# Optimization experiments

Hardware: AMD Instinct MI355X
Metric: run time of the kernel (lower is better)

## Reference

```python
import jax, jax.numpy as jnp
import numpy as np

B, S, H = 32, 2048, 1024

def setup_inputs() -> dict:
    key = jax.random.key(0)
    ks = jax.random.split(key, 8)
    scale = 1.0 / np.sqrt(H)
    return {
        "decoder_hidden": jax.random.normal(ks[0], (B, 1, H), dtype=jnp.float32),
        "encoder_outputs": jax.random.normal(ks[1], (B, S, H), dtype=jnp.float32),
        "coverage": jax.random.uniform(ks[2], (B, S), dtype=jnp.float32),
        "W_enc": jax.random.normal(ks[3], (H, H), dtype=jnp.float32) * scale,  # enc_v.weight [out,in]
        "W_dec": jax.random.normal(ks[4], (H, H), dtype=jnp.float32) * scale,  # dec_v.weight
        "b_dec": jax.random.normal(ks[5], (H,), dtype=jnp.float32) * scale,    # dec_v.bias
        "w_cov": jax.random.normal(ks[6], (H,), dtype=jnp.float32) * scale,    # cov_v.weight [H,1] squeezed
        "v": jax.random.normal(ks[7], (H,), dtype=jnp.float32) * scale,        # V_prime.weight [1,H] squeezed
    }

def reference(decoder_hidden, encoder_outputs, coverage, W_enc, W_dec, b_dec, w_cov, v):
    # enc_feature: [B,S,H]; torch Linear is x @ W.T
    enc_feature = jnp.einsum("bsh,oh->bso", encoder_outputs, W_enc)
    # dec_feature: [B,1,H], broadcasts over S
    dec_feature = jnp.einsum("bqh,oh->bqo", decoder_hidden, W_dec) + b_dec
    # cov_feature: coverage[...,None] @ w_cov[None,:] -> [B,S,H]
    cov_feature = coverage[..., None] * w_cov
    scores = jnp.tanh(enc_feature + dec_feature + cov_feature)  # [B,S,H]
    attn_scores = jnp.einsum("bsh,h->bs", scores, v)            # V_prime, squeeze(-1)
    attn_dist = jax.nn.softmax(attn_scores, axis=-1)[:, None, :]  # [B,1,S]
    return attn_dist
```

## Files before the change

### kernel.cpp

```cpp
#include <hip/hip_runtime.h>
#include <hip/hip_bf16.h>

#define Bb 32
#define Ss 2048
#define Hh 1024

typedef __attribute__((ext_vector_type(4))) float f32x4;
typedef __attribute__((ext_vector_type(8))) short s16x8;

#define GAS const __attribute__((address_space(1))) unsigned int
#define LAS __attribute__((address_space(3))) unsigned int

__device__ __forceinline__ unsigned short f2bf(float x) {
  unsigned int u = __float_as_uint(x);
  u = (u + 0x7fffu + ((u >> 16) & 1u)) >> 16;
  return (unsigned short)u;
}

__global__ void cvt_w_kernel(const float* __restrict__ W, unsigned short* __restrict__ out) {
  int g = blockIdx.x * blockDim.x + threadIdx.x;
  int o = g >> 7;
  int kc8 = (g & 127) << 3;
  const float4* src = reinterpret_cast<const float4*>(W + (size_t)o * Hh + kc8);
  float4 a = src[0], b = src[1];
  union { unsigned short u[8]; uint4 q; } rr;
  rr.u[0] = f2bf(a.x); rr.u[1] = f2bf(a.y); rr.u[2] = f2bf(a.z); rr.u[3] = f2bf(a.w);
  rr.u[4] = f2bf(b.x); rr.u[5] = f2bf(b.y); rr.u[6] = f2bf(b.z); rr.u[7] = f2bf(b.w);
  int ot = o >> 8, r = o & 255, kt = kc8 >> 6, kc = kc8 & 63;
  size_t byte = (size_t)(ot * 16 + kt) * 32768 + (size_t)((r * 128 + kc * 2) ^ ((r & 7) << 4));
  *reinterpret_cast<uint4*>(reinterpret_cast<char*>(out) + byte) = rr.q;
}

__global__ void dec_feat_kernel(const float* __restrict__ dh,
                                const float* __restrict__ Wd,
                                const float* __restrict__ bd,
                                float* __restrict__ out) {
  int gw = blockIdx.x * 4 + (threadIdx.x >> 6);
  int lane = threadIdx.x & 63;
  int b = gw >> 10;
  int o = gw & 1023;
  const float4* x = reinterpret_cast<const float4*>(dh + (size_t)b * Hh);
  const float4* w = reinterpret_cast<const float4*>(Wd + (size_t)o * Hh);
  float acc = 0.f;
#pragma unroll
  for (int it = 0; it < 4; ++it) {
    float4 xa = x[lane + it * 64];
    float4 wa = w[lane + it * 64];
    acc += xa.x * wa.x + xa.y * wa.y + xa.z * wa.z + xa.w * wa.w;
  }
#pragma unroll
  for (int m = 1; m < 64; m <<= 1) acc += __shfl_xor(acc, m, 64);
  if (lane == 0) out[gw] = acc + bd[o];
}

__global__ void __launch_bounds__(512, 2)
gemm_fused(const float* __restrict__ A,
           const unsigned short* __restrict__ Bw,
           const float* __restrict__ decf,
           const float* __restrict__ cov,
           const float* __restrict__ wcov,
           const float* __restrict__ v,
           float* __restrict__ scores) {
  __shared__ uint4 lds_v[8192];
  char* lds = reinterpret_cast<char*>(lds_v);

  int bid = blockIdx.x;
  int swz = (bid & 7) * 128 + (bid >> 3);
  const int s_tile = swz >> 2;
  const int ot = swz & 3;

  const int tid = threadIdx.x;
  const int lane = tid & 63;
  const int wid = tid >> 6;
  const int wm = wid >> 2, wn = wid & 3;
  const int fr = lane & 15, hi = lane >> 4;

  const int arow = tid >> 3, apc = tid & 7;
  const float* gA = A + (size_t)(s_tile * 256 + arow) * 1024 + apc * 8;
  const int aswz = (arow & 7) << 4;

  const char* gB = reinterpret_cast<const char*>(Bw) + (size_t)ot * 16 * 32768 + tid * 16;

  const int fswz = (fr & 7) << 4;
  const int aFragBase = (wm * 128 + fr) * 128 + hi * 16;
  const int bFragBase = 32768 + (wn * 64 + fr) * 128 + hi * 16;

  f32x4 acc[8][4];
#pragma unroll
  for (int i = 0; i < 8; ++i)
#pragma unroll
    for (int j = 0; j < 4; ++j) acc[i][j] = (f32x4){0.f, 0.f, 0.f, 0.f};

  float4 sa[4][2];

#define GLOAD_A(kt) do {                                                         \
    const float* _p = gA + (size_t)(kt) * 64;                                    \
    _Pragma("unroll") for (int i = 0; i < 4; ++i) {                              \
      sa[i][0] = *reinterpret_cast<const float4*>(_p + (size_t)i * 65536);       \
      sa[i][1] = *reinterpret_cast<const float4*>(_p + (size_t)i * 65536 + 4);   \
    }                                                                            \
  } while (0)

#define GLOAD_B(kt, b) do {                                                      \
    _Pragma("unroll") for (int i = 0; i < 4; ++i)                                \
      __builtin_amdgcn_global_load_lds((GAS*)(gB + (size_t)(kt) * 32768 + i * 8192), \
          (LAS*)(lds + (b) * 65536 + 32768 + i * 8192 + tid * 16), 16, 0, 0);    \
  } while (0)

#define AWRITE(b) do {                                                           \
    _Pragma("unroll") for (int i = 0; i < 4; ++i) {                              \
      union { unsigned short u[8]; uint4 q; } w;                                 \
      float4 x = sa[i][0], y = sa[i][1];                                         \
      w.u[0] = f2bf(x.x); w.u[1] = f2bf(x.y); w.u[2] = f2bf(x.z); w.u[3] = f2bf(x.w); \
      w.u[4] = f2bf(y.x); w.u[5] = f2bf(y.y); w.u[6] = f2bf(y.z); w.u[7] = f2bf(y.w); \
      int _byte = (((i * 64 + arow) * 128 + apc * 16) ^ aswz);                   \
      *reinterpret_cast<uint4*>(lds + (b) * 65536 + _byte) = w.q;                \
    }                                                                            \
  } while (0)

#define COMPUTE(b) do {                                                          \
    const char* Lb = lds + (b) * 65536;                                          \
    s16x8 bfr[4][2];                                                             \
    _Pragma("unroll") for (int fn = 0; fn < 4; ++fn)                             \
      _Pragma("unroll") for (int ks = 0; ks < 2; ++ks)                           \
        bfr[fn][ks] = *reinterpret_cast<const s16x8*>(                           \
            Lb + ((bFragBase + fn * 2048 + ks * 64) ^ fswz));                    \
    _Pragma("unroll") for (int mh = 0; mh < 2; ++mh) {                           \
      s16x8 af[4][2];                                                            \
      _Pragma("unroll") for (int fm = 0; fm < 4; ++fm)                           \
        _Pragma("unroll") for (int ks = 0; ks < 2; ++ks)                         \
          af[fm][ks] = *reinterpret_cast<const s16x8*>(                          \
              Lb + ((aFragBase + (mh * 4 + fm) * 2048 + ks * 64) ^ fswz));       \
      _Pragma("unroll") for (int fm = 0; fm < 4; ++fm)                           \
        _Pragma("unroll") for (int fn = 0; fn < 4; ++fn)                         \
          _Pragma("unroll") for (int ks = 0; ks < 2; ++ks)                       \
            acc[mh * 4 + fm][fn] = __builtin_amdgcn_mfma_f32_16x16x32_bf16(      \
                af[fm][ks], bfr[fn][ks], acc[mh * 4 + fm][fn], 0, 0, 0);         \
    }                                                                            \
  } while (0)

  GLOAD_A(0);
  GLOAD_B(0, 0);
  AWRITE(0);
  __syncthreads();

  for (int t = 0; t < 16; ++t) {
    int b = t & 1;
    if (t < 15) {
      GLOAD_A(t + 1);
      GLOAD_B(t + 1, b ^ 1);
    }
    COMPUTE(b);
    if (t < 15) AWRITE(b ^ 1);
    __syncthreads();
  }

#undef GLOAD_A
#undef GLOAD_B
#undef AWRITE
#undef COMPUTE

  const int row0 = s_tile * 256 + wm * 128 + hi * 4;
  const int o0 = ot * 256 + wn * 64 + fr;
  const int bb = s_tile >> 3;

  float vv[4], wv[4], dv[4];
#pragma unroll
  for (int fn = 0; fn < 4; ++fn) {
    int o = o0 + fn * 16;
    vv[fn] = v[o];
    wv[fn] = wcov[o];
    dv[fn] = decf[bb * 1024 + o];
  }

#pragma unroll
  for (int fm = 0; fm < 8; ++fm) {
#pragma unroll
    for (int r = 0; r < 4; ++r) {
      int s_flat = row0 + fm * 16 + r;
      float c = cov[s_flat];
      float sum = 0.f;
#pragma unroll
      for (int fn = 0; fn < 4; ++fn) {
        float x = acc[fm][fn][r] + dv[fn] + c * wv[fn];
        sum += tanhf(x) * vv[fn];
      }
      sum += __shfl_xor(sum, 1, 64);
      sum += __shfl_xor(sum, 2, 64);
      sum += __shfl_xor(sum, 4, 64);
      sum += __shfl_xor(sum, 8, 64);
      if (fr == 0) atomicAdd(&scores[s_flat], sum);
    }
  }
}

__global__ void softmax_kernel(const float* __restrict__ scores, float* __restrict__ out) {
  int b = blockIdx.x;
  int tid = threadIdx.x;
  int lane = tid & 63, w = tid >> 6;
  const float* row = scores + (size_t)b * Ss;
  float vals[8];
#pragma unroll
  for (int k = 0; k < 8; ++k) vals[k] = row[tid + k * 256];
  float m = vals[0];
#pragma unroll
  for (int k = 1; k < 8; ++k) m = fmaxf(m, vals[k]);
#pragma unroll
  for (int off = 1; off < 64; off <<= 1) m = fmaxf(m, __shfl_xor(m, off, 64));
  __shared__ float sm[4], ss[4];
  if (lane == 0) sm[w] = m;
  __syncthreads();
  m = fmaxf(fmaxf(sm[0], sm[1]), fmaxf(sm[2], sm[3]));
  float s = 0.f;
#pragma unroll
  for (int k = 0; k < 8; ++k) { vals[k] = __expf(vals[k] - m); s += vals[k]; }
#pragma unroll
  for (int off = 1; off < 64; off <<= 1) s += __shfl_xor(s, off, 64);
  if (lane == 0) ss[w] = s;
  __syncthreads();
  s = ss[0] + ss[1] + ss[2] + ss[3];
  float inv = 1.f / s;
#pragma unroll
  for (int k = 0; k < 8; ++k) out[(size_t)b * Ss + tid + k * 256] = vals[k] * inv;
}

extern "C" void kernel_launch(void* const* d_in, const int* in_sizes, int n_in,
                              void* d_out, int out_size, void* d_ws, size_t ws_size,
                              hipStream_t stream) {
  const float* dh    = (const float*)d_in[0];
  const float* enc   = (const float*)d_in[1];
  const float* cov   = (const float*)d_in[2];
  const float* W_enc = (const float*)d_in[3];
  const float* W_dec = (const float*)d_in[4];
  const float* b_dec = (const float*)d_in[5];
  const float* w_cov = (const float*)d_in[6];
  const float* v     = (const float*)d_in[7];
  float* out = (float*)d_out;

  char* ws = (char*)d_ws;
  unsigned short* Wswz = (unsigned short*)ws;
  float*          decf = (float*)(ws + 2097152);
  float*          score = (float*)(ws + 2097152 + 131072);

  hipMemsetAsync(score, 0, (size_t)Bb * Ss * sizeof(float), stream);
  cvt_w_kernel<<<512, 256, 0, stream>>>(W_enc, Wswz);
  dec_feat_kernel<<<(Bb * Hh) / 4, 256, 0, stream>>>(dh, W_dec, b_dec, decf);
  gemm_fused<<<1024, 512, 0, stream>>>(enc, Wswz, decf, cov, w_cov, v, score);
  softmax_kernel<<<Bb, 256, 0, stream>>>(score, out);
}
```

Before: 290.5 us.

## Pre-convert encoder outputs to swizzled bf16 and use 4-stage direct-to-LDS GEMM pipeline

Adds a separate pass that converts the fp32 encoder outputs to bf16 in a tiled, swizzled layout, so the GEMM loads both operands with global_load_lds instead of staging A through registers. The GEMM now uses a K-step of 32 with a 4-buffer LDS ring, two phases per step, explicit vmcnt waits, barriers and setprio around the MFMA bursts. The aim is to remove the register round-trip and in-loop conversion on A and overlap loads with compute. In exchange it adds a full extra read of the 256 MB fp32 input plus a 128 MB bf16 write and re-read, and 128 KB of LDS per block, which may lower occupancy.

```diff
diff --git a/kernel.cpp b/kernel.cpp
--- a/kernel.cpp
+++ b/kernel.cpp
@@ -1,5 +1,4 @@
 #include <hip/hip_runtime.h>
-#include <hip/hip_bf16.h>
 
 #define Bb 32
 #define Ss 2048
@@ -17,17 +16,18 @@
   return (unsigned short)u;
 }
 
-__global__ void cvt_w_kernel(const float* __restrict__ W, unsigned short* __restrict__ out) {
+__global__ void cvt_swz_kernel(const float* __restrict__ in, unsigned short* __restrict__ out) {
   int g = blockIdx.x * blockDim.x + threadIdx.x;
-  int o = g >> 7;
+  int row = g >> 7;
   int kc8 = (g & 127) << 3;
-  const float4* src = reinterpret_cast<const float4*>(W + (size_t)o * Hh + kc8);
+  const float4* src = reinterpret_cast<const float4*>(in + (size_t)row * Hh + kc8);
   float4 a = src[0], b = src[1];
   union { unsigned short u[8]; uint4 q; } rr;
   rr.u[0] = f2bf(a.x); rr.u[1] = f2bf(a.y); rr.u[2] = f2bf(a.z); rr.u[3] = f2bf(a.w);
   rr.u[4] = f2bf(b.x); rr.u[5] = f2bf(b.y); rr.u[6] = f2bf(b.z); rr.u[7] = f2bf(b.w);
-  int ot = o >> 8, r = o & 255, kt = kc8 >> 6, kc = kc8 & 63;
-  size_t byte = (size_t)(ot * 16 + kt) * 32768 + (size_t)((r * 128 + kc * 2) ^ ((r & 7) << 4));
+  int r = row & 255;
+  size_t byte = ((size_t)(row >> 8) * 32 + (kc8 >> 5)) * 16384
+              + (size_t)(r * 64 + (((kc8 & 31) * 2) ^ ((r & 3) << 4)));
   *reinterpret_cast<uint4*>(reinterpret_cast<char*>(out) + byte) = rr.q;
 }
 
@@ -54,36 +54,47 @@
 }
 
 __global__ void __launch_bounds__(512, 2)
-gemm_fused(const float* __restrict__ A,
-           const unsigned short* __restrict__ Bw,
-           const float* __restrict__ decf,
-           const float* __restrict__ cov,
-           const float* __restrict__ wcov,
-           const float* __restrict__ v,
-           float* __restrict__ scores) {
-  __shared__ uint4 lds_v[8192];
-  char* lds = reinterpret_cast<char*>(lds_v);
-
-  int bid = blockIdx.x;
-  int swz = (bid & 7) * 128 + (bid >> 3);
+gemm8(const unsigned short* __restrict__ Aw,
+      const unsigned short* __restrict__ Bw,
+      const float* __restrict__ decf,
+      const float* __restrict__ cov,
+      const float* __restrict__ wcov,
+      const float* __restrict__ v,
+      float* __restrict__ scores) {
+  __shared__ char lds[131072];
+
+  const int bid = blockIdx.x;
+  const int swz = (bid & 7) * 128 + (bid >> 3);
   const int s_tile = swz >> 2;
   const int ot = swz & 3;
 
-  const int tid = threadIdx.x;
-  const int lane = tid & 63;
-  const int wid = tid >> 6;
-  const int wm = wid >> 2, wn = wid & 3;
+  const int tid = threadIdx.x, lane = tid & 63;
+  const int wid = tid >> 6, wm = wid >> 2, wn = wid & 3;
   const int fr = lane & 15, hi = lane >> 4;
 
-  const int arow = tid >> 3, apc = tid & 7;
-  const float* gA = A + (size_t)(s_tile * 256 + arow) * 1024 + apc * 8;
-  const int aswz = (arow & 7) << 4;
-
-  const char* gB = reinterpret_cast<const char*>(Bw) + (size_t)ot * 16 * 32768 + tid * 16;
-
-  const int fswz = (fr & 7) << 4;
-  const int aFragBase = (wm * 128 + fr) * 128 + hi * 16;
-  const int bFragBase = 32768 + (wn * 64 + fr) * 128 + hi * 16;
+  const char* gA = reinterpret_cast<const char*>(Aw) + (size_t)s_tile * 32 * 16384 + tid * 16;
+  const char* gB = reinterpret_cast<const char*>(Bw) + (size_t)ot * 32 * 16384 + tid * 16;
+
+#define STAGE_A(t) do {                                                           \
+    const char* _s = gA + (size_t)(t) * 16384;                                    \
+    char* _d = lds + ((t) & 3) * 32768 + tid * 16;                                \
+    __builtin_amdgcn_global_load_lds((GAS*)(_s),        (LAS*)(_d),        16, 0, 0); \
+    __builtin_amdgcn_global_load_lds((GAS*)(_s + 8192), (LAS*)(_d + 8192), 16, 0, 0); \
+  } while (0)
+#define STAGE_B(t) do {                                                           \
+    const char* _s = gB + (size_t)(t) * 16384;                                    \
+    char* _d = lds + ((t) & 3) * 32768 + 16384 + tid * 16;                        \
+    __builtin_amdgcn_global_load_lds((GAS*)(_s),        (LAS*)(_d),        16, 0, 0); \
+    __builtin_amdgcn_global_load_lds((GAS*)(_s + 8192), (LAS*)(_d + 8192), 16, 0, 0); \
+  } while (0)
+#define NOSTAGE ((void)0)
+#define VM4 asm volatile("s_waitcnt vmcnt(4)" ::: "memory")
+#define VM0 asm volatile("s_waitcnt vmcnt(0)" ::: "memory")
+#define NOWAIT ((void)0)
+
+  const int xr = (fr & 3) << 4;
+  const int aOff = wm * 8192 + fr * 64 + ((hi * 16) ^ xr);
+  const int bOff = 16384 + wn * 4096 + fr * 64 + ((hi * 16) ^ xr);
 
   f32x4 acc[8][4];
 #pragma unroll
@@ -91,74 +102,63 @@
 #pragma unroll
     for (int j = 0; j < 4; ++j) acc[i][j] = (f32x4){0.f, 0.f, 0.f, 0.f};
 
-  float4 sa[4][2];
-
-#define GLOAD_A(kt) do {                                                         \
-    const float* _p = gA + (size_t)(kt) * 64;                                    \
-    _Pragma("unroll") for (int i = 0; i < 4; ++i) {                              \
-      sa[i][0] = *reinterpret_cast<const float4*>(_p + (size_t)i * 65536);       \
-      sa[i][1] = *reinterpret_cast<const float4*>(_p + (size_t)i * 65536 + 4);   \
-    }                                                                            \
-  } while (0)
-
-#define GLOAD_B(kt, b) do {                                                      \
-    _Pragma("unroll") for (int i = 0; i < 4; ++i)                                \
-      __builtin_amdgcn_global_load_lds((GAS*)(gB + (size_t)(kt) * 32768 + i * 8192), \
-          (LAS*)(lds + (b) * 65536 + 32768 + i * 8192 + tid * 16), 16, 0, 0);    \
-  } while (0)
-
-#define AWRITE(b) do {                                                           \
-    _Pragma("unroll") for (int i = 0; i < 4; ++i) {                              \
-      union { unsigned short u[8]; uint4 q; } w;                                 \
-      float4 x = sa[i][0], y = sa[i][1];                                         \
-      w.u[0] = f2bf(x.x); w.u[1] = f2bf(x.y); w.u[2] = f2bf(x.z); w.u[3] = f2bf(x.w); \
-      w.u[4] = f2bf(y.x); w.u[5] = f2bf(y.y); w.u[6] = f2bf(y.z); w.u[7] = f2bf(y.w); \
-      int _byte = (((i * 64 + arow) * 128 + apc * 16) ^ aswz);                   \
-      *reinterpret_cast<uint4*>(lds + (b) * 65536 + _byte) = w.q;                \
-    }                                                                            \
-  } while (0)
-
-#define COMPUTE(b) do {                                                          \
-    const char* Lb = lds + (b) * 65536;                                          \
-    s16x8 bfr[4][2];                                                             \
-    _Pragma("unroll") for (int fn = 0; fn < 4; ++fn)                             \
-      _Pragma("unroll") for (int ks = 0; ks < 2; ++ks)                           \
-        bfr[fn][ks] = *reinterpret_cast<const s16x8*>(                           \
-            Lb + ((bFragBase + fn * 2048 + ks * 64) ^ fswz));                    \
-    _Pragma("unroll") for (int mh = 0; mh < 2; ++mh) {                           \
-      s16x8 af[4][2];                                                            \
-      _Pragma("unroll") for (int fm = 0; fm < 4; ++fm)                           \
-        _Pragma("unroll") for (int ks = 0; ks < 2; ++ks)                         \
-          af[fm][ks] = *reinterpret_cast<const s16x8*>(                          \
-              Lb + ((aFragBase + (mh * 4 + fm) * 2048 + ks * 64) ^ fswz));       \
-      _Pragma("unroll") for (int fm = 0; fm < 4; ++fm)                           \
-        _Pragma("unroll") for (int fn = 0; fn < 4; ++fn)                         \
-          _Pragma("unroll") for (int ks = 0; ks < 2; ++ks)                       \
-            acc[mh * 4 + fm][fn] = __builtin_amdgcn_mfma_f32_16x16x32_bf16(      \
-                af[fm][ks], bfr[fn][ks], acc[mh * 4 + fm][fn], 0, 0, 0);         \
-    }                                                                            \
-  } while (0)
-
-  GLOAD_A(0);
-  GLOAD_B(0, 0);
-  AWRITE(0);
-  __syncthreads();
-
-  for (int t = 0; t < 16; ++t) {
-    int b = t & 1;
-    if (t < 15) {
-      GLOAD_A(t + 1);
-      GLOAD_B(t + 1, b ^ 1);
-    }
-    COMPUTE(b);
-    if (t < 15) AWRITE(b ^ 1);
-    __syncthreads();
-  }
-
-#undef GLOAD_A
-#undef GLOAD_B
-#undef AWRITE
-#undef COMPUTE
+  s16x8 afrag[4], bfrag[4];
+
+#define PH_A(t, STAGE) do {                                                       \
+    const char* Lb = lds + ((t) & 3) * 32768;                                     \
+    _Pragma("unroll") for (int fn = 0; fn < 4; ++fn)                              \
+      bfrag[fn] = *reinterpret_cast<const s16x8*>(Lb + bOff + fn * 1024);         \
+    _Pragma("unroll") for (int fm = 0; fm < 4; ++fm)                              \
+      afrag[fm] = *reinterpret_cast<const s16x8*>(Lb + aOff + fm * 1024);         \
+    STAGE;                                                                        \
+    __builtin_amdgcn_s_barrier();                                                 \
+    asm volatile("s_waitcnt lgkmcnt(0)" ::: "memory");                            \
+    __builtin_amdgcn_sched_barrier(0);                                            \
+    __builtin_amdgcn_s_setprio(1);                                                \
+    _Pragma("unroll") for (int fm = 0; fm < 4; ++fm)                              \
+      _Pragma("unroll") for (int fn = 0; fn < 4; ++fn)                            \
+        acc[fm][fn] = __builtin_amdgcn_mfma_f32_16x16x32_bf16(                    \
+            afrag[fm], bfrag[fn], acc[fm][fn], 0, 0, 0);                          \
+    __builtin_amdgcn_s_setprio(0);                                                \
+    __builtin_amdgcn_s_barrier();                                                 \
+  } while (0)
+
+#define PH_B(t, STAGE, WAIT) do {                                                 \
+    const char* Lb = lds + ((t) & 3) * 32768;                                     \
+    _Pragma("unroll") for (int fm = 0; fm < 4; ++fm)                              \
+      afrag[fm] = *reinterpret_cast<const s16x8*>(Lb + aOff + (fm + 4) * 1024);   \
+    STAGE;                                                                        \
+    WAIT;                                                                         \
+    __builtin_amdgcn_s_barrier();                                                 \
+    asm volatile("s_waitcnt lgkmcnt(0)" ::: "memory");                            \
+    __builtin_amdgcn_sched_barrier(0);                                            \
+    __builtin_amdgcn_s_setprio(1);                                                \
+    _Pragma("unroll") for (int fm = 0; fm < 4; ++fm)                              \
+      _Pragma("unroll") for (int fn = 0; fn < 4; ++fn)                            \
+        acc[fm + 4][fn] = __builtin_amdgcn_mfma_f32_16x16x32_bf16(                \
+            afrag[fm], bfrag[fn], acc[fm + 4][fn], 0, 0, 0);                      \
+    __builtin_amdgcn_s_setprio(0);                                                \
+    __builtin_amdgcn_s_barrier();                                                 \
+  } while (0)
+
+  STAGE_A(0); STAGE_B(0);
+  STAGE_A(1); STAGE_B(1);
+  VM4;
+  __builtin_amdgcn_s_barrier();
+
+  for (int t = 0; t < 30; ++t) {
+    PH_A(t, STAGE_A(t + 2));
+    PH_B(t, STAGE_B(t + 2), VM4);
+  }
+  PH_A(30, NOSTAGE);
+  PH_B(30, NOSTAGE, VM0);
+  PH_A(31, NOSTAGE);
+  PH_B(31, NOSTAGE, NOWAIT);
+
+#undef PH_A
+#undef PH_B
+#undef STAGE_A
+#undef STAGE_B
 
   const int row0 = s_tile * 256 + wm * 128 + hi * 4;
   const int o0 = ot * 256 + wn * 64 + fr;
@@ -238,13 +238,15 @@
   float* out = (float*)d_out;
 
   char* ws = (char*)d_ws;
-  unsigned short* Wswz = (unsigned short*)ws;
-  float*          decf = (float*)(ws + 2097152);
-  float*          score = (float*)(ws + 2097152 + 131072);
+  unsigned short* A_bf  = (unsigned short*)ws;
+  unsigned short* W_bf  = (unsigned short*)(ws + 134217728);
+  float*          decf  = (float*)(ws + 136314880);
+  float*          score = (float*)(ws + 136445952);
 
   hipMemsetAsync(score, 0, (size_t)Bb * Ss * sizeof(float), stream);
-  cvt_w_kernel<<<512, 256, 0, stream>>>(W_enc, Wswz);
+  cvt_swz_kernel<<<32768, 256, 0, stream>>>(enc, A_bf);
+  cvt_swz_kernel<<<512, 256, 0, stream>>>(W_enc, W_bf);
   dec_feat_kernel<<<(Bb * Hh) / 4, 256, 0, stream>>>(dh, W_dec, b_dec, decf);
-  gemm_fused<<<1024, 512, 0, stream>>>(enc, Wswz, decf, cov, w_cov, v, score);
+  gemm8<<<1024, 512, 0, stream>>>(A_bf, W_bf, decf, cov, w_cov, v, score);
   softmax_kernel<<<Bb, 256, 0, stream>>>(score, out);
 }
```

After: 304.4 us. +4.8%, slower.

## Load fp32 A tiles directly to LDS and convert at fragment read with smaller tiles

Applied to the files above, without the earlier changes.

The fused GEMM now stages fp32 encoder rows straight into LDS with global_load_lds, instead of loading them into registers and converting to bf16 before the LDS write. Conversion to bf16 happens when fragments are read from LDS. Tiles shrink from 256x256 with 512 threads to 128x128 with 256 threads and a K-step of 32, and the weight swizzle layout is changed to match. tanhf is replaced by an exp-based formula with clamping. The aim is to drop register staging and VALU conversion from the load path and raise occupancy, at the cost of more LDS traffic for fp32 A, fourfold more blocks re-reading the weights, and more atomics.

```diff
diff --git a/kernel.cpp b/kernel.cpp
--- a/kernel.cpp
+++ b/kernel.cpp
@@ -15,6 +15,12 @@
   unsigned int u = __float_as_uint(x);
   u = (u + 0x7fffu + ((u >> 16) & 1u)) >> 16;
   return (unsigned short)u;
+}
+
+__device__ __forceinline__ unsigned short f2bf_n(float x) {
+  union { __hip_bfloat16 h; unsigned short u; } c;
+  c.h = __float2bfloat16(x);
+  return c.u;
 }
 
 __global__ void cvt_w_kernel(const float* __restrict__ W, unsigned short* __restrict__ out) {
@@ -26,8 +32,9 @@
   union { unsigned short u[8]; uint4 q; } rr;
   rr.u[0] = f2bf(a.x); rr.u[1] = f2bf(a.y); rr.u[2] = f2bf(a.z); rr.u[3] = f2bf(a.w);
   rr.u[4] = f2bf(b.x); rr.u[5] = f2bf(b.y); rr.u[6] = f2bf(b.z); rr.u[7] = f2bf(b.w);
-  int ot = o >> 8, r = o & 255, kt = kc8 >> 6, kc = kc8 & 63;
-  size_t byte = (size_t)(ot * 16 + kt) * 32768 + (size_t)((r * 128 + kc * 2) ^ ((r & 7) << 4));
+  int ot = o >> 7, r = o & 127, kt = kc8 >> 5, k0 = kc8 & 31;
+  size_t byte = (size_t)(ot * 32 + kt) * 8192
+              + (size_t)(r * 64 + ((2 * k0) ^ (((r >> 1) & 3) << 4)));
   *reinterpret_cast<uint4*>(reinterpret_cast<char*>(out) + byte) = rr.q;
 }
 
@@ -53,7 +60,7 @@
   if (lane == 0) out[gw] = acc + bd[o];
 }
 
-__global__ void __launch_bounds__(512, 2)
+__global__ void __launch_bounds__(256, 2)
 gemm_fused(const float* __restrict__ A,
            const unsigned short* __restrict__ Bw,
            const float* __restrict__ decf,
@@ -61,108 +68,79 @@
            const float* __restrict__ wcov,
            const float* __restrict__ v,
            float* __restrict__ scores) {
-  __shared__ uint4 lds_v[8192];
-  char* lds = reinterpret_cast<char*>(lds_v);
-
-  int bid = blockIdx.x;
-  int swz = (bid & 7) * 128 + (bid >> 3);
-  const int s_tile = swz >> 2;
-  const int ot = swz & 3;
+  __shared__ char lds[49152];
+
+  const int bid = blockIdx.x;
+  const int swz = (bid & 7) * 512 + (bid >> 3);
+  const int s_tile = swz >> 3;
+  const int o_tile = swz & 7;
 
   const int tid = threadIdx.x;
   const int lane = tid & 63;
   const int wid = tid >> 6;
-  const int wm = wid >> 2, wn = wid & 3;
+  const int wr = wid >> 1, wc = wid & 1;
   const int fr = lane & 15, hi = lane >> 4;
 
-  const int arow = tid >> 3, apc = tid & 7;
-  const float* gA = A + (size_t)(s_tile * 256 + arow) * 1024 + apc * 8;
-  const int aswz = (arow & 7) << 4;
-
-  const char* gB = reinterpret_cast<const char*>(Bw) + (size_t)ot * 16 * 32768 + tid * 16;
-
-  const int fswz = (fr & 7) << 4;
-  const int aFragBase = (wm * 128 + fr) * 128 + hi * 16;
-  const int bFragBase = 32768 + (wn * 64 + fr) * 128 + hi * 16;
-
-  f32x4 acc[8][4];
-#pragma unroll
-  for (int i = 0; i < 8; ++i)
+  const int fr_l = lane >> 3, s8 = lane & 7;
+  const float* gA0 = A + (size_t)(s_tile * 128 + wid * 32 + fr_l) * 1024 + ((s8 ^ fr_l) << 2);
+  const char* gB0 = reinterpret_cast<const char*>(Bw) + (size_t)o_tile * 262144 + tid * 16;
+
+#define STAGE(b, kt) do {                                                          \
+    char* _dA = lds + (b) * 24576 + wid * 4096 + lane * 16;                        \
+    const float* _sA = gA0 + (size_t)(kt) * 32;                                    \
+    _Pragma("unroll") for (int i = 0; i < 4; ++i)                                  \
+      __builtin_amdgcn_global_load_lds((GAS*)(_sA + (size_t)i * 8192),             \
+                                       (LAS*)(_dA + i * 1024), 16, 0, 0);          \
+    char* _dB = lds + (b) * 24576 + 16384 + tid * 16;                              \
+    const char* _sB = gB0 + (size_t)(kt) * 8192;                                   \
+    _Pragma("unroll") for (int i = 0; i < 2; ++i)                                  \
+      __builtin_amdgcn_global_load_lds((GAS*)(_sB + i * 4096),                     \
+                                       (LAS*)(_dB + i * 4096), 16, 0, 0);          \
+  } while (0)
+
+  const int xrA = (fr & 7) << 4;
+  const int xrB = ((fr >> 1) & 3) << 4;
+  const int aBase = (wr * 64 + fr) * 128;
+  const int bBase = 16384 + (wc * 64 + fr) * 64;
+
+  f32x4 acc[4][4];
+#pragma unroll
+  for (int i = 0; i < 4; ++i)
 #pragma unroll
     for (int j = 0; j < 4; ++j) acc[i][j] = (f32x4){0.f, 0.f, 0.f, 0.f};
 
-  float4 sa[4][2];
-
-#define GLOAD_A(kt) do {                                                         \
-    const float* _p = gA + (size_t)(kt) * 64;                                    \
-    _Pragma("unroll") for (int i = 0; i < 4; ++i) {                              \
-      sa[i][0] = *reinterpret_cast<const float4*>(_p + (size_t)i * 65536);       \
-      sa[i][1] = *reinterpret_cast<const float4*>(_p + (size_t)i * 65536 + 4);   \
-    }                                                                            \
-  } while (0)
-
-#define GLOAD_B(kt, b) do {                                                      \
-    _Pragma("unroll") for (int i = 0; i < 4; ++i)                                \
-      __builtin_amdgcn_global_load_lds((GAS*)(gB + (size_t)(kt) * 32768 + i * 8192), \
-          (LAS*)(lds + (b) * 65536 + 32768 + i * 8192 + tid * 16), 16, 0, 0);    \
-  } while (0)
-
-#define AWRITE(b) do {                                                           \
-    _Pragma("unroll") for (int i = 0; i < 4; ++i) {                              \
-      union { unsigned short u[8]; uint4 q; } w;                                 \
-      float4 x = sa[i][0], y = sa[i][1];                                         \
-      w.u[0] = f2bf(x.x); w.u[1] = f2bf(x.y); w.u[2] = f2bf(x.z); w.u[3] = f2bf(x.w); \
-      w.u[4] = f2bf(y.x); w.u[5] = f2bf(y.y); w.u[6] = f2bf(y.z); w.u[7] = f2bf(y.w); \
-      int _byte = (((i * 64 + arow) * 128 + apc * 16) ^ aswz);                   \
-      *reinterpret_cast<uint4*>(lds + (b) * 65536 + _byte) = w.q;                \
-    }                                                                            \
-  } while (0)
-
-#define COMPUTE(b) do {                                                          \
-    const char* Lb = lds + (b) * 65536;                                          \
-    s16x8 bfr[4][2];                                                             \
-    _Pragma("unroll") for (int fn = 0; fn < 4; ++fn)                             \
-      _Pragma("unroll") for (int ks = 0; ks < 2; ++ks)                           \
-        bfr[fn][ks] = *reinterpret_cast<const s16x8*>(                           \
-            Lb + ((bFragBase + fn * 2048 + ks * 64) ^ fswz));                    \
-    _Pragma("unroll") for (int mh = 0; mh < 2; ++mh) {                           \
-      s16x8 af[4][2];                                                            \
-      _Pragma("unroll") for (int fm = 0; fm < 4; ++fm)                           \
-        _Pragma("unroll") for (int ks = 0; ks < 2; ++ks)                         \
-          af[fm][ks] = *reinterpret_cast<const s16x8*>(                          \
-              Lb + ((aFragBase + (mh * 4 + fm) * 2048 + ks * 64) ^ fswz));       \
-      _Pragma("unroll") for (int fm = 0; fm < 4; ++fm)                           \
-        _Pragma("unroll") for (int fn = 0; fn < 4; ++fn)                         \
-          _Pragma("unroll") for (int ks = 0; ks < 2; ++ks)                       \
-            acc[mh * 4 + fm][fn] = __builtin_amdgcn_mfma_f32_16x16x32_bf16(      \
-                af[fm][ks], bfr[fn][ks], acc[mh * 4 + fm][fn], 0, 0, 0);         \
-    }                                                                            \
-  } while (0)
-
-  GLOAD_A(0);
-  GLOAD_B(0, 0);
-  AWRITE(0);
+  STAGE(0, 0);
   __syncthreads();
-
-  for (int t = 0; t < 16; ++t) {
-    int b = t & 1;
-    if (t < 15) {
-      GLOAD_A(t + 1);
-      GLOAD_B(t + 1, b ^ 1);
+  int buf = 0;
+
+  for (int kt = 0; kt < 32; ++kt) {
+    if (kt < 31) STAGE(buf ^ 1, kt + 1);
+    const char* Lb = lds + buf * 24576;
+    s16x8 bfrag[4];
+#pragma unroll
+    for (int fn = 0; fn < 4; ++fn)
+      bfrag[fn] = *reinterpret_cast<const s16x8*>(Lb + bBase + fn * 1024 + ((hi * 16) ^ xrB));
+#pragma unroll
+    for (int fm = 0; fm < 4; ++fm) {
+      f32x4 a0 = *reinterpret_cast<const f32x4*>(Lb + aBase + fm * 2048 + ((hi * 32) ^ xrA));
+      f32x4 a1 = *reinterpret_cast<const f32x4*>(Lb + aBase + fm * 2048 + ((hi * 32 + 16) ^ xrA));
+      union { unsigned short u[8]; s16x8 v; } af;
+      af.u[0] = f2bf_n(a0[0]); af.u[1] = f2bf_n(a0[1]);
+      af.u[2] = f2bf_n(a0[2]); af.u[3] = f2bf_n(a0[3]);
+      af.u[4] = f2bf_n(a1[0]); af.u[5] = f2bf_n(a1[1]);
+      af.u[6] = f2bf_n(a1[2]); af.u[7] = f2bf_n(a1[3]);
+#pragma unroll
+      for (int fn = 0; fn < 4; ++fn)
+        acc[fm][fn] = __builtin_amdgcn_mfma_f32_16x16x32_bf16(af.v, bfrag[fn], acc[fm][fn], 0, 0, 0);
     }
-    COMPUTE(b);
-    if (t < 15) AWRITE(b ^ 1);
     __syncthreads();
-  }
-
-#undef GLOAD_A
-#undef GLOAD_B
-#undef AWRITE
-#undef COMPUTE
-
-  const int row0 = s_tile * 256 + wm * 128 + hi * 4;
-  const int o0 = ot * 256 + wn * 64 + fr;
-  const int bb = s_tile >> 3;
+    buf ^= 1;
+  }
+#undef STAGE
+
+  const int row0 = s_tile * 128 + wr * 64 + hi * 4;
+  const int o0 = o_tile * 128 + wc * 64 + fr;
+  const int bb = s_tile >> 4;
 
   float vv[4], wv[4], dv[4];
 #pragma unroll
@@ -174,7 +152,7 @@
   }
 
 #pragma unroll
-  for (int fm = 0; fm < 8; ++fm) {
+  for (int fm = 0; fm < 4; ++fm) {
 #pragma unroll
     for (int r = 0; r < 4; ++r) {
       int s_flat = row0 + fm * 16 + r;
@@ -183,7 +161,9 @@
 #pragma unroll
       for (int fn = 0; fn < 4; ++fn) {
         float x = acc[fm][fn][r] + dv[fn] + c * wv[fn];
-        sum += tanhf(x) * vv[fn];
+        float xc = fminf(fmaxf(x, -15.f), 15.f);
+        float e2 = __expf(2.f * xc);
+        sum += (1.f - 2.f / (e2 + 1.f)) * vv[fn];
       }
       sum += __shfl_xor(sum, 1, 64);
       sum += __shfl_xor(sum, 2, 64);
@@ -245,6 +225,6 @@
   hipMemsetAsync(score, 0, (size_t)Bb * Ss * sizeof(float), stream);
   cvt_w_kernel<<<512, 256, 0, stream>>>(W_enc, Wswz);
   dec_feat_kernel<<<(Bb * Hh) / 4, 256, 0, stream>>>(dh, W_dec, b_dec, decf);
-  gemm_fused<<<1024, 512, 0, stream>>>(enc, Wswz, decf, cov, w_cov, v, score);
+  gemm_fused<<<4096, 256, 0, stream>>>(enc, Wswz, decf, cov, w_cov, v, score);
   softmax_kernel<<<Bb, 256, 0, stream>>>(score, out);
 }
```

New measurement: 250.3 us. 13.8% less time.
